# Performance work log

Measured on AMD Instinct MI355X. Metric: run time of the kernel, lower is better.

Reference implementation:

```python
import jax, jax.numpy as jnp
import numpy as np

K = 4
KS = 7
SHIFT = KS // 2

def setup_inputs() -> dict:
    key = jax.random.key(0)
    ks = jax.random.split(key, 5)
    B, C, H, W = 8, 128, 256, 256
    x = jax.random.normal(ks[0], (B, C, H, W), dtype=jnp.float32)
    guidance = jax.random.normal(ks[1], (B, C, H, W), dtype=jnp.float32)
    basis_filters = jax.random.normal(ks[2], (K, C, KS, KS), dtype=jnp.float32)
    w1 = jax.random.normal(ks[3], (C // 4, C), dtype=jnp.float32) * (1.0 / np.sqrt(C))
    b1 = jnp.zeros((C // 4,), dtype=jnp.float32)
    w2 = jax.random.normal(ks[4], (K, C // 4), dtype=jnp.float32) * (1.0 / np.sqrt(C // 4))
    b2 = jnp.zeros((K,), dtype=jnp.float32)
    return {"x": x, "guidance": guidance, "basis_filters": basis_filters,
            "w1": w1, "b1": b1, "w2": w2, "b2": b2}

def reference(x, guidance, basis_filters, w1, b1, w2, b2):
    B, C, H, W = x.shape
    # guidance vector: global average pool -> MLP -> softmax over k bases
    g = jnp.mean(guidance, axis=(2, 3))                      # [B, C]
    h1 = jax.nn.relu(g @ w1.T + b1)                          # [B, C//4]
    weights = jax.nn.softmax(h1 @ w2.T + b2, axis=1)         # [B, K]
    # dynamic per-sample depthwise kernel: weighted sum of bases
    dyn = jnp.einsum('bk,kcij->bcij', weights, basis_filters)  # [B, C, KS, KS]
    # pad kernel to full (H, W) at the bottom/right, then roll to center at origin
    padded = jnp.pad(dyn, ((0, 0), (0, 0), (0, H - KS), (0, W - KS)))
    centered = jnp.roll(padded, shift=(-SHIFT, -SHIFT), axis=(-2, -1))
    # circular depthwise convolution via FFT
    filt_fft = jnp.fft.rfft2(centered, s=(H, W), axes=(-2, -1))
    x_fft = jnp.fft.rfft2(x, s=(H, W), axes=(-2, -1))
    out = jnp.fft.irfft2(x_fft * filt_fft, s=(H, W), axes=(-2, -1))
    return out
```

## Files before the change

kernel.cpp:

```cpp
#include <hip/hip_runtime.h>

#define HW 256
#define HWMASK 255
#define CH 128
#define BATCH 8
#define NK 4
#define TS 64
#define LDQ 19

__device__ __forceinline__ int swz(int q, int s) { return q < 16 ? (q ^ s) : q; }
__device__ __forceinline__ int srow(int r) { return ((r >> 2) + r) & 7; }

__global__ __launch_bounds__(256) void mean1_kernel(const float* __restrict__ guid,
                                                    float* __restrict__ partial) {
    int blk = blockIdx.x;
    const float4* p = (const float4*)(guid + (size_t)blk * 16384);
    float s = 0.f;
    for (int i = threadIdx.x; i < 4096; i += 256) {
        float4 v = p[i];
        s += (v.x + v.y) + (v.z + v.w);
    }
    for (int off = 32; off; off >>= 1) s += __shfl_down(s, off, 64);
    __shared__ float red[4];
    if ((threadIdx.x & 63) == 0) red[threadIdx.x >> 6] = s;
    __syncthreads();
    if (threadIdx.x == 0) partial[blk] = (red[0] + red[1]) + (red[2] + red[3]);
}

__global__ __launch_bounds__(256) void mean2_kernel(const float* __restrict__ partial,
                                                    float* __restrict__ g) {
    int bc = blockIdx.x * 256 + threadIdx.x;
    float4 v = *(const float4*)(partial + bc * 4);
    g[bc] = ((v.x + v.y) + (v.z + v.w)) * (1.0f / 65536.0f);
}

__global__ __launch_bounds__(256) void mlp_kernel(const float* __restrict__ g,
                                                  const float* __restrict__ w1,
                                                  const float* __restrict__ b1,
                                                  const float* __restrict__ w2,
                                                  const float* __restrict__ b2,
                                                  float* __restrict__ wt) {
    __shared__ float gs[BATCH * CH];
    __shared__ float h1[BATCH * 32];
    __shared__ float lg[BATCH * NK];
    int t = threadIdx.x;
    for (int i = t; i < BATCH * CH; i += 256) gs[i] = g[i];
    __syncthreads();
    {
        int b = t >> 5, j = t & 31;
        float acc = b1[j];
        #pragma unroll 4
        for (int c = 0; c < CH; ++c) acc += gs[b * CH + c] * w1[j * CH + c];
        h1[b * 32 + j] = fmaxf(acc, 0.f);
    }
    __syncthreads();
    if (t < BATCH * NK) {
        int b = t >> 2, k = t & 3;
        float acc = b2[k];
        #pragma unroll
        for (int j = 0; j < 32; ++j) acc += h1[b * 32 + j] * w2[k * 32 + j];
        lg[b * NK + k] = acc;
    }
    __syncthreads();
    if (t < BATCH) {
        int b = t;
        float m = lg[b * 4];
        for (int k = 1; k < 4; ++k) m = fmaxf(m, lg[b * 4 + k]);
        float e[4], s = 0.f;
        for (int k = 0; k < 4; ++k) { e[k] = expf(lg[b * 4 + k] - m); s += e[k]; }
        float inv = 1.0f / s;
        for (int k = 0; k < 4; ++k) wt[b * 4 + k] = e[k] * inv;
    }
}

__global__ __launch_bounds__(256) void dyn_kernel(const float* __restrict__ wt,
                                                  const float* __restrict__ basis,
                                                  float* __restrict__ dynF) {
    int idx = blockIdx.x * 256 + threadIdx.x;
    if (idx >= BATCH * CH * 49) return;
    int ij = idx % 49;
    int bc = idx / 49;
    int c = bc % CH;
    int b = bc / CH;
    float acc = 0.f;
    #pragma unroll
    for (int k = 0; k < NK; ++k)
        acc += wt[b * NK + k] * basis[(k * CH + c) * 49 + ij];
    dynF[bc * 49 + (48 - ij)] = acc;
}

__global__ __launch_bounds__(256) void conv_kernel(const float* __restrict__ x,
                                                   const float* __restrict__ dynF,
                                                   float* __restrict__ out) {
    int bc = blockIdx.z;
    int x0 = blockIdx.x * TS;
    int y0 = blockIdx.y * TS;
    __shared__ float4 lds4[70 * LDQ];
    const float* xp = x + (size_t)bc * (HW * HW);

    const float* df = dynF + bc * 49;
    float d[49];
    #pragma unroll
    for (int i = 0; i < 49; ++i) d[i] = df[i];

    int tid = threadIdx.x;
    int c4 = tid % 18, r0 = tid / 18;
    if (r0 < 14) {
        int gx = (x0 - 4 + 4 * c4) & HWMASK;
        #pragma unroll
        for (int k = 0; k < 5; ++k) {
            int r = r0 + 14 * k;
            int gy = (y0 + r - 3) & HWMASK;
            float4 v = *(const float4*)(xp + gy * HW + gx);
            lds4[r * LDQ + swz(c4, srow(r))] = v;
        }
    }
    __syncthreads();

    int tx = tid & 15, ty = tid >> 4;
    int lx0 = tx * 4, ly0 = ty * 4;
    float acc[4][4] = {};
    #pragma unroll
    for (int rr = 0; rr < 10; ++rr) {
        int r = ly0 + rr;
        int s = srow(r);
        int rb = r * LDQ;
        float4 A  = lds4[rb + swz(tx,     s)];
        float4 Bv = lds4[rb + swz(tx + 1, s)];
        float4 Cv = lds4[rb + swz(tx + 2, s)];
        float v[12] = {A.x, A.y, A.z, A.w,
                       Bv.x, Bv.y, Bv.z, Bv.w,
                       Cv.x, Cv.y, Cv.z, Cv.w};
        #pragma unroll
        for (int rq = 0; rq < 4; ++rq) {
            int ii = rr - rq;
            if (ii >= 0 && ii <= 6) {
                #pragma unroll
                for (int q = 0; q < 4; ++q) {
                    #pragma unroll
                    for (int jj = 0; jj < 7; ++jj)
                        acc[rq][q] += d[ii * 7 + jj] * v[q + 1 + jj];
                }
            }
        }
    }
    float* op = out + (size_t)bc * (HW * HW);
    #pragma unroll
    for (int rq = 0; rq < 4; ++rq) {
        float4 o = {acc[rq][0], acc[rq][1], acc[rq][2], acc[rq][3]};
        *(float4*)&op[(y0 + ly0 + rq) * HW + x0 + lx0] = o;
    }
}

extern "C" void kernel_launch(void* const* d_in, const int* in_sizes, int n_in,
                              void* d_out, int out_size, void* d_ws, size_t ws_size,
                              hipStream_t stream) {
    const float* x        = (const float*)d_in[0];
    const float* guidance = (const float*)d_in[1];
    const float* basis    = (const float*)d_in[2];
    const float* w1       = (const float*)d_in[3];
    const float* b1       = (const float*)d_in[4];
    const float* w2       = (const float*)d_in[5];
    const float* b2       = (const float*)d_in[6];
    float* out = (float*)d_out;
    float* ws  = (float*)d_ws;

    float* g       = ws;
    float* wt      = ws + 1024;
    float* dynF    = ws + 1024 + 32;
    float* partial = ws + 51232;

    mean1_kernel<<<4096, 256, 0, stream>>>(guidance, partial);
    mean2_kernel<<<4, 256, 0, stream>>>(partial, g);
    mlp_kernel<<<1, 256, 0, stream>>>(g, w1, b1, w2, b2, wt);
    dyn_kernel<<<(BATCH * CH * 49 + 255) / 256, 256, 0, stream>>>(wt, basis, dynF);
    conv_kernel<<<dim3(HW / TS, HW / TS, BATCH * CH), 256, 0, stream>>>(x, dynF, out);
}
```

Measured before the change: 208.2 us.

## Widen conv tile to 128x64 with 8 outputs per thread; fold mean2 into MLP

The depthwise conv tile widens from 64x64 to 128x64, and each thread now computes 4x8 outputs instead of 4x4. This cuts the halo overhead per output and reuses each loaded LDS row across more outputs. The LDS layout and swizzle are widened to match, and the cooperative load now loops over 70x34 float4 elements. Separately, the mean2 kernel is folded into the MLP kernel, removing one launch. The cost is more accumulator registers per thread, which may lower occupancy, and half as many conv blocks.

```diff
diff --git a/kernel.cpp b/kernel.cpp
--- a/kernel.cpp
+++ b/kernel.cpp
@@ -5,11 +5,13 @@
 #define CH 128
 #define BATCH 8
 #define NK 4
-#define TS 64
-#define LDQ 19
+#define TSX 128
+#define TSY 64
+#define LDQ 35
+#define NQ 34
 
-__device__ __forceinline__ int swz(int q, int s) { return q < 16 ? (q ^ s) : q; }
 __device__ __forceinline__ int srow(int r) { return ((r >> 2) + r) & 7; }
+__device__ __forceinline__ int wswz(int q, int s) { return q < 32 ? (q ^ s) : q; }
 
 __global__ __launch_bounds__(256) void mean1_kernel(const float* __restrict__ guid,
                                                     float* __restrict__ partial) {
@@ -27,14 +29,7 @@
     if (threadIdx.x == 0) partial[blk] = (red[0] + red[1]) + (red[2] + red[3]);
 }
 
-__global__ __launch_bounds__(256) void mean2_kernel(const float* __restrict__ partial,
-                                                    float* __restrict__ g) {
-    int bc = blockIdx.x * 256 + threadIdx.x;
-    float4 v = *(const float4*)(partial + bc * 4);
-    g[bc] = ((v.x + v.y) + (v.z + v.w)) * (1.0f / 65536.0f);
-}
-
-__global__ __launch_bounds__(256) void mlp_kernel(const float* __restrict__ g,
+__global__ __launch_bounds__(256) void mlp_kernel(const float* __restrict__ partial,
                                                   const float* __restrict__ w1,
                                                   const float* __restrict__ b1,
                                                   const float* __restrict__ w2,
@@ -44,7 +39,10 @@
     __shared__ float h1[BATCH * 32];
     __shared__ float lg[BATCH * NK];
     int t = threadIdx.x;
-    for (int i = t; i < BATCH * CH; i += 256) gs[i] = g[i];
+    for (int i = t; i < BATCH * CH; i += 256) {
+        float4 v = *(const float4*)(partial + i * 4);
+        gs[i] = ((v.x + v.y) + (v.z + v.w)) * (1.0f / 65536.0f);
+    }
     __syncthreads();
     {
         int b = t >> 5, j = t & 31;
@@ -93,8 +91,8 @@
                                                    const float* __restrict__ dynF,
                                                    float* __restrict__ out) {
     int bc = blockIdx.z;
-    int x0 = blockIdx.x * TS;
-    int y0 = blockIdx.y * TS;
+    int x0 = blockIdx.x * TSX;
+    int y0 = blockIdx.y * TSY;
     __shared__ float4 lds4[70 * LDQ];
     const float* xp = x + (size_t)bc * (HW * HW);
 
@@ -104,51 +102,59 @@
     for (int i = 0; i < 49; ++i) d[i] = df[i];
 
     int tid = threadIdx.x;
-    int c4 = tid % 18, r0 = tid / 18;
-    if (r0 < 14) {
-        int gx = (x0 - 4 + 4 * c4) & HWMASK;
+    {
+        int e = tid;
+        int r = e / NQ;
+        int c = e - r * NQ;
         #pragma unroll
-        for (int k = 0; k < 5; ++k) {
-            int r = r0 + 14 * k;
-            int gy = (y0 + r - 3) & HWMASK;
-            float4 v = *(const float4*)(xp + gy * HW + gx);
-            lds4[r * LDQ + swz(c4, srow(r))] = v;
+        for (int it = 0; it < 10; ++it) {
+            if (e < 70 * NQ) {
+                int gy = (y0 + r - 3) & HWMASK;
+                int gx = (x0 + 4 * c - 4) & HWMASK;
+                float4 v = *(const float4*)(xp + gy * HW + gx);
+                lds4[r * LDQ + wswz(c, srow(r))] = v;
+            }
+            e += 256; c += 18; r += 7;
+            if (c >= NQ) { c -= NQ; r += 1; }
         }
     }
     __syncthreads();
 
     int tx = tid & 15, ty = tid >> 4;
-    int lx0 = tx * 4, ly0 = ty * 4;
-    float acc[4][4] = {};
+    int lx0 = 8 * tx, ly0 = 4 * ty;
+    float acc[4][8] = {};
     #pragma unroll
     for (int rr = 0; rr < 10; ++rr) {
         int r = ly0 + rr;
         int s = srow(r);
         int rb = r * LDQ;
-        float4 A  = lds4[rb + swz(tx,     s)];
-        float4 Bv = lds4[rb + swz(tx + 1, s)];
-        float4 Cv = lds4[rb + swz(tx + 2, s)];
-        float v[12] = {A.x, A.y, A.z, A.w,
-                       Bv.x, Bv.y, Bv.z, Bv.w,
-                       Cv.x, Cv.y, Cv.z, Cv.w};
+        float4 A = lds4[rb + wswz(2 * tx,     s)];
+        float4 B = lds4[rb + wswz(2 * tx + 1, s)];
+        float4 C = lds4[rb + wswz(2 * tx + 2, s)];
+        float4 D = lds4[rb + wswz(2 * tx + 3, s)];
+        float v[16] = {A.x, A.y, A.z, A.w, B.x, B.y, B.z, B.w,
+                       C.x, C.y, C.z, C.w, D.x, D.y, D.z, D.w};
         #pragma unroll
         for (int rq = 0; rq < 4; ++rq) {
             int ii = rr - rq;
             if (ii >= 0 && ii <= 6) {
                 #pragma unroll
-                for (int q = 0; q < 4; ++q) {
+                for (int q = 0; q < 8; ++q) {
                     #pragma unroll
                     for (int jj = 0; jj < 7; ++jj)
-                        acc[rq][q] += d[ii * 7 + jj] * v[q + 1 + jj];
+                        acc[rq][q] += d[ii * 7 + jj] * v[q + jj + 1];
                 }
             }
         }
     }
-    float* op = out + (size_t)bc * (HW * HW);
+    float* op = out + (size_t)bc * (HW * HW) + x0 + lx0;
     #pragma unroll
     for (int rq = 0; rq < 4; ++rq) {
-        float4 o = {acc[rq][0], acc[rq][1], acc[rq][2], acc[rq][3]};
-        *(float4*)&op[(y0 + ly0 + rq) * HW + x0 + lx0] = o;
+        float4 o0 = {acc[rq][0], acc[rq][1], acc[rq][2], acc[rq][3]};
+        float4 o1 = {acc[rq][4], acc[rq][5], acc[rq][6], acc[rq][7]};
+        float* row = op + (y0 + ly0 + rq) * HW;
+        *(float4*)(row)     = o0;
+        *(float4*)(row + 4) = o1;
     }
 }
 
@@ -165,14 +171,12 @@
     float* out = (float*)d_out;
     float* ws  = (float*)d_ws;
 
-    float* g       = ws;
-    float* wt      = ws + 1024;
-    float* dynF    = ws + 1024 + 32;
-    float* partial = ws + 51232;
+    float* partial = ws;
+    float* wt      = ws + 4096;
+    float* dynF    = ws + 4096 + 32;
 
     mean1_kernel<<<4096, 256, 0, stream>>>(guidance, partial);
-    mean2_kernel<<<4, 256, 0, stream>>>(partial, g);
-    mlp_kernel<<<1, 256, 0, stream>>>(g, w1, b1, w2, b2, wt);
+    mlp_kernel<<<1, 256, 0, stream>>>(partial, w1, b1, w2, b2, wt);
     dyn_kernel<<<(BATCH * CH * 49 + 255) / 256, 256, 0, stream>>>(wt, basis, dynF);
-    conv_kernel<<<dim3(HW / TS, HW / TS, BATCH * CH), 256, 0, stream>>>(x, dynF, out);
+    conv_kernel<<<dim3(HW / TSX, HW / TSY, BATCH * CH), 256, 0, stream>>>(x, dynF, out);
 }
```

Measured after the change: 208.8 us. About the same (+0.3%).
